# Optimization experiments

Measured on AMD Instinct MI355X. Metric: run time of the kernel, lower is better.

Reference implementation:

```python
import jax, jax.numpy as jnp
import numpy as np

D = 256      # d_model
NH = 8       # heads
NL = 3       # layers
DFF = 1024   # ffn hidden
WIN = 64     # attention window
EPS = 1e-5


def _sin_pos_embed(L, d):
    # Sinusoidal positional embedding, matches _create_pos_embedding.
    pos = jnp.arange(L, dtype=jnp.float32)[:, None]
    div = jnp.exp(jnp.arange(0, d, 2, dtype=jnp.float32) * (-np.log(10000.0) / d))
    pe = jnp.zeros((L, d), jnp.float32)
    pe = pe.at[:, 0::2].set(jnp.sin(pos * div))
    pe = pe.at[:, 1::2].set(jnp.cos(pos * div))
    return pe  # [L, D]


def _layer_norm(x, scale, bias):
    m = jnp.mean(x, axis=-1, keepdims=True)
    v = jnp.mean(jnp.square(x - m), axis=-1, keepdims=True)
    return (x - m) * jax.lax.rsqrt(v + EPS) * scale + bias


def _mha(x, Wi, bi, Wo, bo):
    # x: [N, S, D]; Wi: [3D, D]; Wo: [D, D]. torch nn.MultiheadAttention semantics (eval, no dropout).
    N, S, _ = x.shape
    dh = D // NH
    qkv = x @ Wi.T + bi                       # [N, S, 3D]
    q, k, v = jnp.split(qkv, 3, axis=-1)
    q = q.reshape(N, S, NH, dh).transpose(0, 2, 1, 3) * (dh ** -0.5)
    k = k.reshape(N, S, NH, dh).transpose(0, 2, 1, 3)
    v = v.reshape(N, S, NH, dh).transpose(0, 2, 1, 3)
    attn = jax.nn.softmax(jnp.einsum('nhqd,nhkd->nhqk', q, k), axis=-1)
    out = jnp.einsum('nhqk,nhkd->nhqd', attn, v)
    out = out.transpose(0, 2, 1, 3).reshape(N, S, D)
    return out @ Wo.T + bo


def setup_inputs() -> dict:
    key = jax.random.key(0)
    ks = jax.random.split(key, 16)
    s = 0.02
    return {
        'features': jax.random.normal(ks[0], (32, D, 32, 32), jnp.float32),
        'in_proj_w': jax.random.normal(ks[1], (NL, 3 * D, D), jnp.float32) * s,
        'in_proj_b': jnp.zeros((NL, 3 * D), jnp.float32),
        'out_proj_w': jax.random.normal(ks[2], (NL, D, D), jnp.float32) * s,
        'out_proj_b': jnp.zeros((NL, D), jnp.float32),
        'w1': jax.random.normal(ks[3], (NL, DFF, D), jnp.float32) * s,
        'b1': jnp.zeros((NL, DFF), jnp.float32),
        'w2': jax.random.normal(ks[4], (NL, D, DFF), jnp.float32) * s,
        'b2': jnp.zeros((NL, D), jnp.float32),
        'ln1_s': jnp.ones((NL, D), jnp.float32),
        'ln1_b': jnp.zeros((NL, D), jnp.float32),
        'ln2_s': jnp.ones((NL, D), jnp.float32),
        'ln2_b': jnp.zeros((NL, D), jnp.float32),
        'fnorm_s': jnp.ones((D,), jnp.float32),
        'fnorm_b': jnp.zeros((D,), jnp.float32),
    }


def reference(features, in_proj_w, in_proj_b, out_proj_w, out_proj_b,
              w1, b1, w2, b2, ln1_s, ln1_b, ln2_s, ln2_b, fnorm_s, fnorm_b):
    B, C, H, W = features.shape
    L = H * W
    x = features.reshape(B, C, L).transpose(0, 2, 1)   # [B, L, D]
    x = x + _sin_pos_embed(L, D)[None]                 # L == 1024 == max_len, no interp
    nw = L // WIN                                      # non-overlapping windows
    for i in range(NL):
        # windowed self-attention: all windows batched in one MHA call
        xw = x.reshape(B * nw, WIN, D)
        att = _mha(xw, in_proj_w[i], in_proj_b[i], out_proj_w[i], out_proj_b[i])
        att = att.reshape(B, L, D)
        x = _layer_norm(x + att, ln1_s[i], ln1_b[i])
        h = jax.nn.gelu(x @ w1[i].T + b1[i], approximate=False) @ w2[i].T + b2[i]
        x = _layer_norm(x + h, ln2_s[i], ln2_b[i])
    x = _layer_norm(x, fnorm_s, fnorm_b)
    return x.transpose(0, 2, 1).reshape(B, C, H, W)
```

## Files before the change

### kernel.cpp

```cpp
#include <hip/hip_runtime.h>
#include <hip/hip_bf16.h>

#define BSZ 32
#define DM 256
#define LSEQ 1024
#define MTOK (BSZ * LSEQ)
#define NHEAD 8
#define DHEAD 32
#define WIN 64
#define DFF 1024
#define M8 ((size_t)MTOK * 8)

typedef short bf16x8 __attribute__((ext_vector_type(8)));
typedef float f32x4 __attribute__((ext_vector_type(4)));
typedef unsigned short u16x8 __attribute__((ext_vector_type(8)));

union BF { __hip_bfloat16 h; unsigned short u; };
__device__ __forceinline__ unsigned short f2bf(float f) { BF b; b.h = __float2bfloat16(f); return b.u; }
__device__ __forceinline__ float bf2f(unsigned short u) { return __uint_as_float((unsigned)u << 16); }

#define GLD_LDS16(gp, lp) __builtin_amdgcn_global_load_lds( \
    (const __attribute__((address_space(1))) void*)(gp),    \
    (__attribute__((address_space(3))) void*)(lp), 16, 0, 0)

__device__ __forceinline__ float gelu_fast(float x) {
    float t = x * (0.7978845608f + 0.0356774081f * x * x);
    return x / (1.0f + __expf(-2.0f * t));
}

__global__ __launch_bounds__(256) void cvt_kernel(
    const float* __restrict__ s, unsigned short* __restrict__ d,
    int N, int K, int nl)
{
    int K8 = K >> 3;
    int per = N * K8;
    int c = blockIdx.x * 256 + threadIdx.x;
    if (c >= per * nl) return;
    int layer = c / per, rem = c - layer * per;
    int n = rem / K8, kc = rem - n * K8;
    const float* sp = s + (size_t)layer * N * K + (size_t)n * K + kc * 8;
    float4 v0 = *(const float4*)sp, v1 = *(const float4*)(sp + 4);
    uint4 o;
    o.x = f2bf(v0.x) | ((unsigned)f2bf(v0.y) << 16);
    o.y = f2bf(v0.z) | ((unsigned)f2bf(v0.w) << 16);
    o.z = f2bf(v1.x) | ((unsigned)f2bf(v1.y) << 16);
    o.w = f2bf(v1.z) | ((unsigned)f2bf(v1.w) << 16);
    *(uint4*)(d + (size_t)layer * N * K + (size_t)kc * N * 8 + (size_t)n * 8) = o;
}

__global__ __launch_bounds__(256) void pe_kernel(float* __restrict__ PE)
{
    int l = blockIdx.x, c = threadIdx.x;
    int i2 = c & ~1;
    float div = expf(-9.210340371976184f * (float)i2 / 256.0f);
    float ang = (float)l * div;
    PE[l * DM + c] = (c & 1) ? cosf(ang) : sinf(ang);
}

__global__ __launch_bounds__(256) void embed_kernel(
    const float* __restrict__ F, const float* __restrict__ PE,
    float* __restrict__ Xf, unsigned short* __restrict__ Xb)
{
    __shared__ float tile[64][65];
    int b = blockIdx.z, l0 = blockIdx.y * 64, c0 = blockIdx.x * 64;
    int tid = threadIdx.x;
    int li = tid & 63, c4 = tid >> 6;
    #pragma unroll
    for (int it = 0; it < 16; ++it) {
        int c = c4 + it * 4;
        tile[c][li] = F[((size_t)(b * DM + c0 + c)) * LSEQ + l0 + li];
    }
    __syncthreads();
    int ci = tid & 63, l4 = tid >> 6;
    #pragma unroll
    for (int it = 0; it < 16; ++it) {
        int l = l4 + it * 4;
        float x = tile[ci][l] + PE[(l0 + l) * DM + c0 + ci];
        Xf[((size_t)b * LSEQ + l0 + l) * DM + c0 + ci] = x;
    }
    int ch = tid >> 5;
    int lx = tid & 31;
    #pragma unroll
    for (int rd = 0; rd < 2; ++rd) {
        int l = lx + rd * 32;
        unsigned short vs[8];
        #pragma unroll
        for (int e = 0; e < 8; ++e) {
            int c = ch * 8 + e;
            vs[e] = f2bf(tile[c][l] + PE[(l0 + l) * DM + c0 + c]);
        }
        uint4 o;
        o.x = vs[0] | ((unsigned)vs[1] << 16);
        o.y = vs[2] | ((unsigned)vs[3] << 16);
        o.z = vs[4] | ((unsigned)vs[5] << 16);
        o.w = vs[6] | ((unsigned)vs[7] << 16);
        *(uint4*)(Xb + ((size_t)((c0 >> 3) + ch)) * M8 +
                  (size_t)(b * LSEQ + l0 + l) * 8) = o;
    }
}

__global__ __launch_bounds__(256) void gemm_mfma_kernel(
    const unsigned short* __restrict__ A, const unsigned short* __restrict__ Bw,
    const float* __restrict__ bias, unsigned short* __restrict__ Cb,
    int M, int N, int K, int gelu)
{
    const int tid = threadIdx.x;
    const int lane = tid & 63, wave = tid >> 6;
    const int l15 = lane & 15, quad = lane >> 4;
    const int wm = (wave & 1) * 64, wn = (wave >> 1) * 64;
    const int m0 = blockIdx.x * 128, n0 = blockIdx.y * 128;
    const size_t Ma8 = (size_t)M * 8, Nb8 = (size_t)N * 8;
    const size_t astep = 4 * Ma8, bstep = 4 * Nb8;

    const unsigned short* ap[4];
    const unsigned short* bp[4];
    #pragma unroll
    for (int i = 0; i < 4; ++i)
        ap[i] = A + quad * Ma8 + (size_t)(m0 + wm + i * 16 + l15) * 8;
    #pragma unroll
    for (int j = 0; j < 4; ++j)
        bp[j] = Bw + quad * Nb8 + (size_t)(n0 + wn + j * 16 + l15) * 8;

    f32x4 acc[4][4] = {};
    bf16x8 aA[4], bA[4], aB[4], bB[4];
    #pragma unroll
    for (int i = 0; i < 4; ++i) aA[i] = *(const bf16x8*)(ap[i]);
    #pragma unroll
    for (int j = 0; j < 4; ++j) bA[j] = *(const bf16x8*)(bp[j]);

    const int iters = K >> 5;
    for (int t = 0; t < iters; t += 2) {
        size_t o1 = (size_t)(t + 1);
        #pragma unroll
        for (int i = 0; i < 4; ++i) aB[i] = *(const bf16x8*)(ap[i] + o1 * astep);
        #pragma unroll
        for (int j = 0; j < 4; ++j) bB[j] = *(const bf16x8*)(bp[j] + o1 * bstep);
        #pragma unroll
        for (int i = 0; i < 4; ++i)
            #pragma unroll
            for (int j = 0; j < 4; ++j)
                acc[i][j] = __builtin_amdgcn_mfma_f32_16x16x32_bf16(
                    bA[j], aA[i], acc[i][j], 0, 0, 0);
        size_t o2 = (size_t)((t + 2 < iters) ? t + 2 : iters - 1);
        #pragma unroll
        for (int i = 0; i < 4; ++i) aA[i] = *(const bf16x8*)(ap[i] + o2 * astep);
        #pragma unroll
        for (int j = 0; j < 4; ++j) bA[j] = *(const bf16x8*)(bp[j] + o2 * bstep);
        #pragma unroll
        for (int i = 0; i < 4; ++i)
            #pragma unroll
            for (int j = 0; j < 4; ++j)
                acc[i][j] = __builtin_amdgcn_mfma_f32_16x16x32_bf16(
                    bB[j], aB[i], acc[i][j], 0, 0, 0);
    }

    float4 bb[4];
    #pragma unroll
    for (int j = 0; j < 4; ++j)
        bb[j] = *(const float4*)(bias + n0 + wn + j * 16 + quad * 4);

    #pragma unroll
    for (int i = 0; i < 4; ++i) {
        const size_t m8 = (size_t)(m0 + wm + i * 16 + l15) * 8;
        #pragma unroll
        for (int j = 0; j < 4; ++j) {
            int nb = n0 + wn + j * 16 + quad * 4;
            float v0 = acc[i][j][0] + bb[j].x;
            float v1 = acc[i][j][1] + bb[j].y;
            float v2 = acc[i][j][2] + bb[j].z;
            float v3 = acc[i][j][3] + bb[j].w;
            if (gelu) {
                v0 = gelu_fast(v0); v1 = gelu_fast(v1);
                v2 = gelu_fast(v2); v3 = gelu_fast(v3);
            }
            uint2 o;
            o.x = f2bf(v0) | ((unsigned)f2bf(v1) << 16);
            o.y = f2bf(v2) | ((unsigned)f2bf(v3) << 16);
            *(uint2*)(Cb + ((size_t)(nb >> 3)) * Ma8 + m8 + (nb & 7)) = o;
        }
    }
}

__global__ __launch_bounds__(256) void gemm_ln_kernel(
    const unsigned short* __restrict__ A, const unsigned short* __restrict__ Bw,
    const float* __restrict__ bias, const float* __restrict__ resid,
    const float* __restrict__ lns, const float* __restrict__ lnb,
    float* __restrict__ Xf, unsigned short* __restrict__ Xb, int K)
{
    __shared__ float Ss[256], Sq[256];
    const int tid = threadIdx.x;
    const int lane = tid & 63, wave = tid >> 6;
    const int l15 = lane & 15, quad = lane >> 4;
    const int wn = wave * 64;
    const int m0 = blockIdx.x * 64;
    const size_t Nb8 = (size_t)DM * 8;
    const size_t astep = 4 * M8, bstep = 4 * Nb8;

    const unsigned short* ap[4];
    const unsigned short* bp[4];
    #pragma unroll
    for (int i = 0; i < 4; ++i)
        ap[i] = A + quad * M8 + (size_t)(m0 + i * 16 + l15) * 8;
    #pragma unroll
    for (int j = 0; j < 4; ++j)
        bp[j] = Bw + quad * Nb8 + (size_t)(wn + j * 16 + l15) * 8;

    f32x4 acc[4][4] = {};
    bf16x8 aA[4], bA[4], aB[4], bB[4];
    #pragma unroll
    for (int i = 0; i < 4; ++i) aA[i] = *(const bf16x8*)(ap[i]);
    #pragma unroll
    for (int j = 0; j < 4; ++j) bA[j] = *(const bf16x8*)(bp[j]);

    const int iters = K >> 5;
    for (int t = 0; t < iters; t += 2) {
        size_t o1 = (size_t)(t + 1);
        #pragma unroll
        for (int i = 0; i < 4; ++i) aB[i] = *(const bf16x8*)(ap[i] + o1 * astep);
        #pragma unroll
        for (int j = 0; j < 4; ++j) bB[j] = *(const bf16x8*)(bp[j] + o1 * bstep);
        #pragma unroll
        for (int i = 0; i < 4; ++i)
            #pragma unroll
            for (int j = 0; j < 4; ++j)
                acc[i][j] = __builtin_amdgcn_mfma_f32_16x16x32_bf16(
                    bA[j], aA[i], acc[i][j], 0, 0, 0);
        size_t o2 = (size_t)((t + 2 < iters) ? t + 2 : iters - 1);
        #pragma unroll
        for (int i = 0; i < 4; ++i) aA[i] = *(const bf16x8*)(ap[i] + o2 * astep);
        #pragma unroll
        for (int j = 0; j < 4; ++j) bA[j] = *(const bf16x8*)(bp[j] + o2 * bstep);
        #pragma unroll
        for (int i = 0; i < 4; ++i)
            #pragma unroll
            for (int j = 0; j < 4; ++j)
                acc[i][j] = __builtin_amdgcn_mfma_f32_16x16x32_bf16(
                    bB[j], aB[i], acc[i][j], 0, 0, 0);
    }

    float4 bj[4];
    #pragma unroll
    for (int j = 0; j < 4; ++j)
        bj[j] = *(const float4*)(bias + wn + j * 16 + quad * 4);
    #pragma unroll
    for (int i = 0; i < 4; ++i) {
        const float* rp = resid + (size_t)(m0 + i * 16 + l15) * DM + wn + quad * 4;
        #pragma unroll
        for (int j = 0; j < 4; ++j) {
            float4 rr = *(const float4*)(rp + j * 16);
            acc[i][j][0] += bj[j].x + rr.x;
            acc[i][j][1] += bj[j].y + rr.y;
            acc[i][j][2] += bj[j].z + rr.z;
            acc[i][j][3] += bj[j].w + rr.w;
        }
    }

    #pragma unroll
    for (int i = 0; i < 4; ++i) {
        float s = 0.f, q = 0.f;
        #pragma unroll
        for (int j = 0; j < 4; ++j)
            #pragma unroll
            for (int r = 0; r < 4; ++r) {
                float x = acc[i][j][r];
                s += x; q = fmaf(x, x, q);
            }
        s += __shfl_xor(s, 16); q += __shfl_xor(q, 16);
        s += __shfl_xor(s, 32); q += __shfl_xor(q, 32);
        if (quad == 0) {
            Ss[wave * 64 + i * 16 + l15] = s;
            Sq[wave * 64 + i * 16 + l15] = q;
        }
    }
    __syncthreads();

    float4 scj[4], bbj[4];
    #pragma unroll
    for (int j = 0; j < 4; ++j) {
        scj[j] = *(const float4*)(lns + wn + j * 16 + quad * 4);
        bbj[j] = *(const float4*)(lnb + wn + j * 16 + quad * 4);
    }
    #pragma unroll
    for (int i = 0; i < 4; ++i) {
        int row = i * 16 + l15;
        float s = Ss[row] + Ss[64 + row] + Ss[128 + row] + Ss[192 + row];
        float q = Sq[row] + Sq[64 + row] + Sq[128 + row] + Sq[192 + row];
        float mean = s * (1.0f / 256.0f);
        float var  = q * (1.0f / 256.0f) - mean * mean;
        float rinv = rsqrtf(var + 1e-5f);
        #pragma unroll
        for (int j = 0; j < 4; ++j) {
            acc[i][j][0] = (acc[i][j][0] - mean) * rinv * scj[j].x + bbj[j].x;
            acc[i][j][1] = (acc[i][j][1] - mean) * rinv * scj[j].y + bbj[j].y;
            acc[i][j][2] = (acc[i][j][2] - mean) * rinv * scj[j].z + bbj[j].z;
            acc[i][j][3] = (acc[i][j][3] - mean) * rinv * scj[j].w + bbj[j].w;
        }
    }

    #pragma unroll
    for (int i = 0; i < 4; ++i) {
        int m = m0 + i * 16 + l15;
        size_t gf = (size_t)m * DM + wn + quad * 4;
        size_t m8 = (size_t)m * 8;
        #pragma unroll
        for (int j = 0; j < 4; ++j) {
            float4 o = { acc[i][j][0], acc[i][j][1], acc[i][j][2], acc[i][j][3] };
            *(float4*)(Xf + gf + j * 16) = o;
            int nb = wn + j * 16 + quad * 4;
            uint2 ob;
            ob.x = f2bf(o.x) | ((unsigned)f2bf(o.y) << 16);
            ob.y = f2bf(o.z) | ((unsigned)f2bf(o.w) << 16);
            *(uint2*)(Xb + ((size_t)(nb >> 3)) * M8 + m8 + (nb & 7)) = ob;
        }
    }
}

__global__ __launch_bounds__(256, 2) void ffn_fused_kernel(
    const unsigned short* __restrict__ A, const unsigned short* __restrict__ W1w,
    const float* __restrict__ b1, const unsigned short* __restrict__ W2w,
    const float* __restrict__ b2, const float* __restrict__ resid,
    const float* __restrict__ lns, const float* __restrict__ lnb,
    float* __restrict__ Xf, unsigned short* __restrict__ Xb)
{
    __shared__ unsigned short Hlds[16384];
    __shared__ float Ss[256], Sq[256];
    const int tid = threadIdx.x;
    const int lane = tid & 63, wave = tid >> 6;
    const int l15 = lane & 15, quad = lane >> 4;
    const int wn = wave * 64;
    const int m0 = blockIdx.x * 64;
    const size_t N1b8 = (size_t)DFF * 8;
    const size_t astep = 4 * M8, b1step = 4 * N1b8;

    const unsigned short* ap[4];
    #pragma unroll
    for (int i = 0; i < 4; ++i)
        ap[i] = A + quad * M8 + (size_t)(m0 + i * 16 + l15) * 8;

    f32x4 acc2[4][4] = {};

    for (int qq = 0; qq < 4; ++qq) {
        const unsigned short* bp[4];
        #pragma unroll
        for (int j = 0; j < 4; ++j)
            bp[j] = W1w + quad * N1b8 + (size_t)(qq * 256 + wn + j * 16 + l15) * 8;

        f32x4 acc1[4][4] = {};
        {
            bf16x8 aA[4], bA[4], aB[4], bB[4];
            #pragma unroll
            for (int i = 0; i < 4; ++i) aA[i] = *(const bf16x8*)(ap[i]);
            #pragma unroll
            for (int j = 0; j < 4; ++j) bA[j] = *(const bf16x8*)(bp[j]);
            for (int t = 0; t < 8; t += 2) {
                size_t o1 = (size_t)(t + 1);
                #pragma unroll
                for (int i = 0; i < 4; ++i) aB[i] = *(const bf16x8*)(ap[i] + o1 * astep);
                #pragma unroll
                for (int j = 0; j < 4; ++j) bB[j] = *(const bf16x8*)(bp[j] + o1 * b1step);
                #pragma unroll
                for (int i = 0; i < 4; ++i)
                    #pragma unroll
                    for (int j = 0; j < 4; ++j)
                        acc1[i][j] = __builtin_amdgcn_mfma_f32_16x16x32_bf16(
                            bA[j], aA[i], acc1[i][j], 0, 0, 0);
                size_t o2 = (size_t)((t + 2 < 8) ? t + 2 : 7);
                #pragma unroll
                for (int i = 0; i < 4; ++i) aA[i] = *(const bf16x8*)(ap[i] + o2 * astep);
                #pragma unroll
                for (int j = 0; j < 4; ++j) bA[j] = *(const bf16x8*)(bp[j] + o2 * b1step);
                #pragma unroll
                for (int i = 0; i < 4; ++i)
                    #pragma unroll
                    for (int j = 0; j < 4; ++j)
                        acc1[i][j] = __builtin_amdgcn_mfma_f32_16x16x32_bf16(
                            bB[j], aB[i], acc1[i][j], 0, 0, 0);
            }
        }
        {
            float4 bb[4];
            #pragma unroll
            for (int j = 0; j < 4; ++j)
                bb[j] = *(const float4*)(b1 + qq * 256 + wn + j * 16 + quad * 4);
            #pragma unroll
            for (int i = 0; i < 4; ++i) {
                int m = i * 16 + l15;
                #pragma unroll
                for (int j = 0; j < 4; ++j) {
                    float v0 = gelu_fast(acc1[i][j][0] + bb[j].x);
                    float v1 = gelu_fast(acc1[i][j][1] + bb[j].y);
                    float v2 = gelu_fast(acc1[i][j][2] + bb[j].z);
                    float v3 = gelu_fast(acc1[i][j][3] + bb[j].w);
                    int chunk = wave * 8 + j * 2 + (quad >> 1);
                    uint2 o;
                    o.x = f2bf(v0) | ((unsigned)f2bf(v1) << 16);
                    o.y = f2bf(v2) | ((unsigned)f2bf(v3) << 16);
                    *(uint2*)(Hlds + chunk * 512 + m * 8 + (quad & 1) * 4) = o;
                }
            }
        }
        __syncthreads();

        {
            const unsigned short* b2p[4];
            #pragma unroll
            for (int j = 0; j < 4; ++j)
                b2p[j] = W2w + ((size_t)(qq * 32 + quad)) * 2048 +
                         (size_t)(wn + j * 16 + l15) * 8;
            bf16x8 hA[4], w2A[4], w2B[4];
            #pragma unroll
            for (int j = 0; j < 4; ++j) w2A[j] = *(const bf16x8*)(b2p[j]);
            for (int t = 0; t < 8; t += 2) {
                size_t o1 = (size_t)(t + 1);
                #pragma unroll
                for (int j = 0; j < 4; ++j)
                    w2B[j] = *(const bf16x8*)(b2p[j] + o1 * 8192);
                #pragma unroll
                for (int i = 0; i < 4; ++i)
                    hA[i] = *(const bf16x8*)(Hlds + (t * 4 + quad) * 512 +
                                             (i * 16 + l15) * 8);
                #pragma unroll
                for (int i = 0; i < 4; ++i)
                    #pragma unroll
                    for (int j = 0; j < 4; ++j)
                        acc2[i][j] = __builtin_amdgcn_mfma_f32_16x16x32_bf16(
                            w2A[j], hA[i], acc2[i][j], 0, 0, 0);
                size_t o2 = (size_t)((t + 2 < 8) ? t + 2 : 7);
                #pragma unroll
                for (int j = 0; j < 4; ++j)
                    w2A[j] = *(const bf16x8*)(b2p[j] + o2 * 8192);
                #pragma unroll
                for (int i = 0; i < 4; ++i)
                    hA[i] = *(const bf16x8*)(Hlds + ((t + 1) * 4 + quad) * 512 +
                                             (i * 16 + l15) * 8);
                #pragma unroll
                for (int i = 0; i < 4; ++i)
                    #pragma unroll
                    for (int j = 0; j < 4; ++j)
                        acc2[i][j] = __builtin_amdgcn_mfma_f32_16x16x32_bf16(
                            w2B[j], hA[i], acc2[i][j], 0, 0, 0);
            }
        }
        __syncthreads();
    }

    float4 bj[4];
    #pragma unroll
    for (int j = 0; j < 4; ++j)
        bj[j] = *(const float4*)(b2 + wn + j * 16 + quad * 4);
    #pragma unroll
    for (int i = 0; i < 4; ++i) {
        const float* rp = resid + (size_t)(m0 + i * 16 + l15) * DM + wn + quad * 4;
        #pragma unroll
        for (int j = 0; j < 4; ++j) {
            float4 rr = *(const float4*)(rp + j * 16);
            acc2[i][j][0] += bj[j].x + rr.x;
            acc2[i][j][1] += bj[j].y + rr.y;
            acc2[i][j][2] += bj[j].z + rr.z;
            acc2[i][j][3] += bj[j].w + rr.w;
        }
    }

    #pragma unroll
    for (int i = 0; i < 4; ++i) {
        float s = 0.f, q = 0.f;
        #pragma unroll
        for (int j = 0; j < 4; ++j)
            #pragma unroll
            for (int r = 0; r < 4; ++r) {
                float x = acc2[i][j][r];
                s += x; q = fmaf(x, x, q);
            }
        s += __shfl_xor(s, 16); q += __shfl_xor(q, 16);
        s += __shfl_xor(s, 32); q += __shfl_xor(q, 32);
        if (quad == 0) {
            Ss[wave * 64 + i * 16 + l15] = s;
            Sq[wave * 64 + i * 16 + l15] = q;
        }
    }
    __syncthreads();

    float4 scj[4], bbj[4];
    #pragma unroll
    for (int j = 0; j < 4; ++j) {
        scj[j] = *(const float4*)(lns + wn + j * 16 + quad * 4);
        bbj[j] = *(const float4*)(lnb + wn + j * 16 + quad * 4);
    }
    #pragma unroll
    for (int i = 0; i < 4; ++i) {
        int row = i * 16 + l15;
        float s = Ss[row] + Ss[64 + row] + Ss[128 + row] + Ss[192 + row];
        float q = Sq[row] + Sq[64 + row] + Sq[128 + row] + Sq[192 + row];
        float mean = s * (1.0f / 256.0f);
        float var  = q * (1.0f / 256.0f) - mean * mean;
        float rinv = rsqrtf(var + 1e-5f);
        #pragma unroll
        for (int j = 0; j < 4; ++j) {
            acc2[i][j][0] = (acc2[i][j][0] - mean) * rinv * scj[j].x + bbj[j].x;
            acc2[i][j][1] = (acc2[i][j][1] - mean) * rinv * scj[j].y + bbj[j].y;
            acc2[i][j][2] = (acc2[i][j][2] - mean) * rinv * scj[j].z + bbj[j].z;
            acc2[i][j][3] = (acc2[i][j][3] - mean) * rinv * scj[j].w + bbj[j].w;
        }
    }

    #pragma unroll
    for (int i = 0; i < 4; ++i) {
        int m = m0 + i * 16 + l15;
        size_t gf = (size_t)m * DM + wn + quad * 4;
        size_t m8 = (size_t)m * 8;
        #pragma unroll
        for (int j = 0; j < 4; ++j) {
            float4 o = { acc2[i][j][0], acc2[i][j][1], acc2[i][j][2], acc2[i][j][3] };
            *(float4*)(Xf + gf + j * 16) = o;
            int nb = wn + j * 16 + quad * 4;
            uint2 ob;
            ob.x = f2bf(o.x) | ((unsigned)f2bf(o.y) << 16);
            ob.y = f2bf(o.z) | ((unsigned)f2bf(o.w) << 16);
            *(uint2*)(Xb + ((size_t)(nb >> 3)) * M8 + m8 + (nb & 7)) = ob;
        }
    }
}

__global__ __launch_bounds__(64) void attn_mfma_kernel(
    const unsigned short* __restrict__ QKV, unsigned short* __restrict__ ATT)
{
    __shared__ __align__(16) char smem[22016];
    unsigned short* Qs = (unsigned short*)smem;
    unsigned short* Ks = (unsigned short*)(smem + 4096);
    unsigned short* VT = (unsigned short*)(smem + 8192);
    unsigned short* Ps = (unsigned short*)(smem + 12800);
    float*          Po = (float*)(smem + 12800);

    const int wg = blockIdx.x, h = blockIdx.y;
    const int base = wg * WIN;
    const int lane = threadIdx.x;
    const int l15 = lane & 15, quad = lane >> 4;
    const float scale = 0.17677669529663687f;

    #pragma unroll
    for (int dc = 0; dc < 4; ++dc) {
        GLD_LDS16(QKV + ((size_t)(h * 4 + dc)) * M8 + (size_t)(base + lane) * 8,
                  Qs + dc * 512 + (size_t)lane * 8);
        GLD_LDS16(QKV + ((size_t)(32 + h * 4 + dc)) * M8 + (size_t)(base + lane) * 8,
                  Ks + dc * 512 + (size_t)lane * 8);
    }
    u16x8 vv[4];
    #pragma unroll
    for (int cc = 0; cc < 4; ++cc)
        vv[cc] = *(const u16x8*)(QKV + ((size_t)(64 + h * 4 + cc)) * M8 +
                                 (size_t)(base + lane) * 8);
    #pragma unroll
    for (int cc = 0; cc < 4; ++cc)
        #pragma unroll
        for (int e = 0; e < 8; ++e)
            VT[(cc * 8 + e) * 72 + lane] = vv[cc][e];
    __syncthreads();

    const f32x4 zero4 = {0.f, 0.f, 0.f, 0.f};
    bf16x8 aq[4], bk[4];
    #pragma unroll
    for (int i = 0; i < 4; ++i)
        aq[i] = *(const bf16x8*)(Qs + quad * 512 + (i * 16 + l15) * 8);
    #pragma unroll
    for (int j = 0; j < 4; ++j)
        bk[j] = *(const bf16x8*)(Ks + quad * 512 + (j * 16 + l15) * 8);
    f32x4 S[4][4];
    #pragma unroll
    for (int i = 0; i < 4; ++i)
        #pragma unroll
        for (int j = 0; j < 4; ++j)
            S[i][j] = __builtin_amdgcn_mfma_f32_16x16x32_bf16(aq[i], bk[j], zero4, 0, 0, 0);

    float mx[4][4], sum[4][4];
    #pragma unroll
    for (int i = 0; i < 4; ++i)
        #pragma unroll
        for (int r = 0; r < 4; ++r) {
            float m0 = -1e30f;
            #pragma unroll
            for (int j = 0; j < 4; ++j) {
                S[i][j][r] *= scale;
                m0 = fmaxf(m0, S[i][j][r]);
            }
            mx[i][r] = m0;
        }
    #pragma unroll
    for (int off = 1; off < 16; off <<= 1)
        #pragma unroll
        for (int i = 0; i < 4; ++i)
            #pragma unroll
            for (int r = 0; r < 4; ++r)
                mx[i][r] = fmaxf(mx[i][r], __shfl_xor(mx[i][r], off));
    #pragma unroll
    for (int i = 0; i < 4; ++i)
        #pragma unroll
        for (int r = 0; r < 4; ++r) {
            float s0 = 0.f;
            #pragma unroll
            for (int j = 0; j < 4; ++j) {
                float e = __expf(S[i][j][r] - mx[i][r]);
                S[i][j][r] = e;
                s0 += e;
            }
            sum[i][r] = s0;
        }
    #pragma unroll
    for (int off = 1; off < 16; off <<= 1)
        #pragma unroll
        for (int i = 0; i < 4; ++i)
            #pragma unroll
            for (int r = 0; r < 4; ++r)
                sum[i][r] += __shfl_xor(sum[i][r], off);

    #pragma unroll
    for (int i = 0; i < 4; ++i)
        #pragma unroll
        for (int r = 0; r < 4; ++r) {
            float inv = 1.0f / sum[i][r];
            #pragma unroll
            for (int j = 0; j < 4; ++j)
                Ps[(i * 16 + quad * 4 + r) * 72 + j * 16 + l15] =
                    f2bf(S[i][j][r] * inv);
        }
    asm volatile("s_waitcnt lgkmcnt(0)" ::: "memory");

    bf16x8 ap0[4], ap1[4], bv0[2], bv1[2];
    #pragma unroll
    for (int i = 0; i < 4; ++i) {
        ap0[i] = *(const bf16x8*)(Ps + (i * 16 + l15) * 72 + quad * 8);
        ap1[i] = *(const bf16x8*)(Ps + (i * 16 + l15) * 72 + 32 + quad * 8);
    }
    #pragma unroll
    for (int jd = 0; jd < 2; ++jd) {
        bv0[jd] = *(const bf16x8*)(VT + (jd * 16 + l15) * 72 + quad * 8);
        bv1[jd] = *(const bf16x8*)(VT + (jd * 16 + l15) * 72 + 32 + quad * 8);
    }
    f32x4 O[4][2];
    #pragma unroll
    for (int i = 0; i < 4; ++i)
        #pragma unroll
        for (int jd = 0; jd < 2; ++jd) {
            f32x4 t = __builtin_amdgcn_mfma_f32_16x16x32_bf16(ap0[i], bv0[jd], zero4, 0, 0, 0);
            O[i][jd] = __builtin_amdgcn_mfma_f32_16x16x32_bf16(ap1[i], bv1[jd], t, 0, 0, 0);
        }
    asm volatile("s_waitcnt lgkmcnt(0)" ::: "memory");

    #pragma unroll
    for (int i = 0; i < 4; ++i)
        #pragma unroll
        for (int jd = 0; jd < 2; ++jd)
            #pragma unroll
            for (int r = 0; r < 4; ++r)
                Po[(i * 16 + quad * 4 + r) * 36 + jd * 16 + l15] = O[i][jd][r];
    asm volatile("s_waitcnt lgkmcnt(0)" ::: "memory");

    #pragma unroll
    for (int g = 0; g < 4; ++g) {
        f32x4 t0 = *(const f32x4*)(Po + lane * 36 + g * 8);
        f32x4 t1 = *(const f32x4*)(Po + lane * 36 + g * 8 + 4);
        uint4 w;
        w.x = f2bf(t0[0]) | ((unsigned)f2bf(t0[1]) << 16);
        w.y = f2bf(t0[2]) | ((unsigned)f2bf(t0[3]) << 16);
        w.z = f2bf(t1[0]) | ((unsigned)f2bf(t1[1]) << 16);
        w.w = f2bf(t1[2]) | ((unsigned)f2bf(t1[3]) << 16);
        *(uint4*)(ATT + ((size_t)(h * 4 + g)) * M8 + (size_t)(base + lane) * 8) = w;
    }
}

__global__ __launch_bounds__(256) void out_ln_kernel(
    const float* __restrict__ Xf, const float* __restrict__ sc,
    const float* __restrict__ bi, float* __restrict__ out)
{
    __shared__ float tile[64][257];
    __shared__ float mean_s[64], rinv_s[64];
    int b = blockIdx.y, l0 = blockIdx.x * 64;
    int tid = threadIdx.x, wave = tid >> 6, lane = tid & 63;
    int c = lane * 4;
    #pragma unroll
    for (int it = 0; it < 16; ++it) {
        int tl = wave * 16 + it;
        float4 v = *(const float4*)(Xf + ((size_t)(b * LSEQ + l0 + tl)) * DM + c);
        *(float4*)&tile[tl][c] = v;
        float sm = v.x + v.y + v.z + v.w;
        float sq = v.x * v.x + v.y * v.y + v.z * v.z + v.w * v.w;
        #pragma unroll
        for (int off = 32; off > 0; off >>= 1) {
            sm += __shfl_down(sm, off);
            sq += __shfl_down(sq, off);
        }
        if (lane == 0) {
            float mean = sm * (1.0f / 256.0f);
            float var  = sq * (1.0f / 256.0f) - mean * mean;
            mean_s[tl] = mean;
            rinv_s[tl] = rsqrtf(var + 1e-5f);
        }
    }
    __syncthreads();
    int lout = tid & 63, crow = tid >> 6;
    #pragma unroll
    for (int ct = 0; ct < 4; ++ct) {
        int c0 = ct * 64;
        #pragma unroll
        for (int it = 0; it < 16; ++it) {
            int cc = c0 + crow + it * 4;
            float v = tile[lout][cc];
            out[((size_t)(b * DM + cc)) * LSEQ + l0 + lout] =
                (v - mean_s[lout]) * rinv_s[lout] * sc[cc] + bi[cc];
        }
    }
}

extern "C" void kernel_launch(void* const* d_in, const int* in_sizes, int n_in,
                              void* d_out, int out_size, void* d_ws, size_t ws_size,
                              hipStream_t stream)
{
    const float* F   = (const float*)d_in[0];
    const float* Wi  = (const float*)d_in[1];
    const float* Bi  = (const float*)d_in[2];
    const float* Wo  = (const float*)d_in[3];
    const float* Bo  = (const float*)d_in[4];
    const float* W1  = (const float*)d_in[5];
    const float* B1  = (const float*)d_in[6];
    const float* W2  = (const float*)d_in[7];
    const float* B2  = (const float*)d_in[8];
    const float* L1s = (const float*)d_in[9];
    const float* L1b = (const float*)d_in[10];
    const float* L2s = (const float*)d_in[11];
    const float* L2b = (const float*)d_in[12];
    const float* Fs  = (const float*)d_in[13];
    const float* Fb  = (const float*)d_in[14];

    char* w = (char*)d_ws;
    float*          Xf   = (float*)w;
    unsigned short* QKVb = (unsigned short*)(w + 33554432);
    unsigned short* Hb   = (unsigned short*)(w + 83886080);
    unsigned short* Xb   = (unsigned short*)(w + 150994944);
    unsigned short* ATTb = (unsigned short*)(w + 167772160);
    unsigned short* WB   = (unsigned short*)(w + 184549376);
    float*          PE   = (float*)(w + 189267968);
    unsigned short* Wib  = WB;
    unsigned short* Wob  = WB + 589824;
    unsigned short* W1b  = WB + 786432;
    unsigned short* W2b  = WB + 1572864;
    (void)Hb;

    cvt_kernel<<<(3 * 768 * 32 + 255) / 256, 256, 0, stream>>>(Wi, Wib, 768, 256, 3);
    cvt_kernel<<<(3 * 256 * 32 + 255) / 256, 256, 0, stream>>>(Wo, Wob, 256, 256, 3);
    cvt_kernel<<<(3 * 1024 * 32 + 255) / 256, 256, 0, stream>>>(W1, W1b, 1024, 256, 3);
    cvt_kernel<<<(3 * 256 * 128 + 255) / 256, 256, 0, stream>>>(W2, W2b, 256, 1024, 3);
    pe_kernel<<<LSEQ, 256, 0, stream>>>(PE);
    embed_kernel<<<dim3(DM / 64, LSEQ / 64, BSZ), 256, 0, stream>>>(F, PE, Xf, Xb);

    for (int i = 0; i < 3; ++i) {
        gemm_mfma_kernel<<<dim3(MTOK / 128, 768 / 128), 256, 0, stream>>>(
            Xb, Wib + (size_t)i * 196608, Bi + i * 768, QKVb, MTOK, 768, DM, 0);
        attn_mfma_kernel<<<dim3(BSZ * (LSEQ / WIN), NHEAD), 64, 0, stream>>>(QKVb, ATTb);
        gemm_ln_kernel<<<MTOK / 64, 256, 0, stream>>>(
            ATTb, Wob + (size_t)i * 65536, Bo + i * DM, Xf,
            L1s + i * DM, L1b + i * DM, Xf, Xb, DM);
        ffn_fused_kernel<<<MTOK / 64, 256, 0, stream>>>(
            Xb, W1b + (size_t)i * 262144, B1 + i * DFF,
            W2b + (size_t)i * 262144, B2 + i * DM, Xf,
            L2s + i * DM, L2b + i * DM, Xf, Xb);
    }

    out_ln_kernel<<<dim3(LSEQ / 64, BSZ), 256, 0, stream>>>(
        Xf, Fs, Fb, (float*)d_out);
}
```

Baseline: 646.3 us.

## Split fused FFN across 8 waves with double-buffered hidden LDS tile

The fused FFN kernel now launches 512 threads: the 64-row tile is split between two wave groups, so each wave holds half as many accumulators. This cuts register pressure and allows more waves per CU to hide global-load latency. The GELU hidden tile in LDS is double-buffered, which removes the second barrier per 256-column chunk. In exchange, the manual A/B register prefetch pipelining is dropped in favour of simple unrolled loops, each wave re-reads the same weight fragments for fewer rows, and LDS use grows.

```diff
diff --git a/kernel.cpp b/kernel.cpp
--- a/kernel.cpp
+++ b/kernel.cpp
@@ -315,87 +315,75 @@
     }
 }
 
-__global__ __launch_bounds__(256, 2) void ffn_fused_kernel(
+__global__ __launch_bounds__(512, 4) void ffn_fused_kernel(
     const unsigned short* __restrict__ A, const unsigned short* __restrict__ W1w,
     const float* __restrict__ b1, const unsigned short* __restrict__ W2w,
     const float* __restrict__ b2, const float* __restrict__ resid,
     const float* __restrict__ lns, const float* __restrict__ lnb,
     float* __restrict__ Xf, unsigned short* __restrict__ Xb)
 {
-    __shared__ unsigned short Hlds[16384];
+    __shared__ unsigned short Hlds[2][16384];
     __shared__ float Ss[256], Sq[256];
     const int tid = threadIdx.x;
     const int lane = tid & 63, wave = tid >> 6;
     const int l15 = lane & 15, quad = lane >> 4;
-    const int wn = wave * 64;
+    const int wh = wave >> 2;
+    const int wq = wave & 3;
+    const int wn = wq * 64;
     const int m0 = blockIdx.x * 64;
     const size_t N1b8 = (size_t)DFF * 8;
     const size_t astep = 4 * M8, b1step = 4 * N1b8;
 
-    const unsigned short* ap[4];
-    #pragma unroll
-    for (int i = 0; i < 4; ++i)
-        ap[i] = A + quad * M8 + (size_t)(m0 + i * 16 + l15) * 8;
-
-    f32x4 acc2[4][4] = {};
+    const unsigned short* ap0 = A + quad * M8 + (size_t)(m0 + wh * 32 + l15) * 8;
+    const unsigned short* ap1 = ap0 + 16 * 8;
+
+    f32x4 acc2[2][4] = {};
 
     for (int qq = 0; qq < 4; ++qq) {
+        unsigned short* Hbuf = Hlds[qq & 1];
         const unsigned short* bp[4];
         #pragma unroll
         for (int j = 0; j < 4; ++j)
             bp[j] = W1w + quad * N1b8 + (size_t)(qq * 256 + wn + j * 16 + l15) * 8;
 
-        f32x4 acc1[4][4] = {};
-        {
-            bf16x8 aA[4], bA[4], aB[4], bB[4];
-            #pragma unroll
-            for (int i = 0; i < 4; ++i) aA[i] = *(const bf16x8*)(ap[i]);
-            #pragma unroll
-            for (int j = 0; j < 4; ++j) bA[j] = *(const bf16x8*)(bp[j]);
-            for (int t = 0; t < 8; t += 2) {
-                size_t o1 = (size_t)(t + 1);
-                #pragma unroll
-                for (int i = 0; i < 4; ++i) aB[i] = *(const bf16x8*)(ap[i] + o1 * astep);
-                #pragma unroll
-                for (int j = 0; j < 4; ++j) bB[j] = *(const bf16x8*)(bp[j] + o1 * b1step);
-                #pragma unroll
-                for (int i = 0; i < 4; ++i)
-                    #pragma unroll
-                    for (int j = 0; j < 4; ++j)
-                        acc1[i][j] = __builtin_amdgcn_mfma_f32_16x16x32_bf16(
-                            bA[j], aA[i], acc1[i][j], 0, 0, 0);
-                size_t o2 = (size_t)((t + 2 < 8) ? t + 2 : 7);
-                #pragma unroll
-                for (int i = 0; i < 4; ++i) aA[i] = *(const bf16x8*)(ap[i] + o2 * astep);
-                #pragma unroll
-                for (int j = 0; j < 4; ++j) bA[j] = *(const bf16x8*)(bp[j] + o2 * b1step);
-                #pragma unroll
-                for (int i = 0; i < 4; ++i)
-                    #pragma unroll
-                    for (int j = 0; j < 4; ++j)
-                        acc1[i][j] = __builtin_amdgcn_mfma_f32_16x16x32_bf16(
-                            bB[j], aB[i], acc1[i][j], 0, 0, 0);
-            }
-        }
+        f32x4 acc1[2][4] = {};
+        #pragma unroll
+        for (int t = 0; t < 8; ++t) {
+            bf16x8 a0 = *(const bf16x8*)(ap0 + (size_t)t * astep);
+            bf16x8 a1 = *(const bf16x8*)(ap1 + (size_t)t * astep);
+            bf16x8 w0 = *(const bf16x8*)(bp[0] + (size_t)t * b1step);
+            bf16x8 w1 = *(const bf16x8*)(bp[1] + (size_t)t * b1step);
+            bf16x8 w2 = *(const bf16x8*)(bp[2] + (size_t)t * b1step);
+            bf16x8 w3 = *(const bf16x8*)(bp[3] + (size_t)t * b1step);
+            acc1[0][0] = __builtin_amdgcn_mfma_f32_16x16x32_bf16(w0, a0, acc1[0][0], 0, 0, 0);
+            acc1[0][1] = __builtin_amdgcn_mfma_f32_16x16x32_bf16(w1, a0, acc1[0][1], 0, 0, 0);
+            acc1[0][2] = __builtin_amdgcn_mfma_f32_16x16x32_bf16(w2, a0, acc1[0][2], 0, 0, 0);
+            acc1[0][3] = __builtin_amdgcn_mfma_f32_16x16x32_bf16(w3, a0, acc1[0][3], 0, 0, 0);
+            acc1[1][0] = __builtin_amdgcn_mfma_f32_16x16x32_bf16(w0, a1, acc1[1][0], 0, 0, 0);
+            acc1[1][1] = __builtin_amdgcn_mfma_f32_16x16x32_bf16(w1, a1, acc1[1][1], 0, 0, 0);
+            acc1[1][2] = __builtin_amdgcn_mfma_f32_16x16x32_bf16(w2, a1, acc1[1][2], 0, 0, 0);
+            acc1[1][3] = __builtin_amdgcn_mfma_f32_16x16x32_bf16(w3, a1, acc1[1][3], 0, 0, 0);
+        }
+
         {
             float4 bb[4];
             #pragma unroll
             for (int j = 0; j < 4; ++j)
                 bb[j] = *(const float4*)(b1 + qq * 256 + wn + j * 16 + quad * 4);
             #pragma unroll
-            for (int i = 0; i < 4; ++i) {
-                int m = i * 16 + l15;
+            for (int i = 0; i < 2; ++i) {
+                int m = wh * 32 + i * 16 + l15;
                 #pragma unroll
                 for (int j = 0; j < 4; ++j) {
                     float v0 = gelu_fast(acc1[i][j][0] + bb[j].x);
                     float v1 = gelu_fast(acc1[i][j][1] + bb[j].y);
                     float v2 = gelu_fast(acc1[i][j][2] + bb[j].z);
                     float v3 = gelu_fast(acc1[i][j][3] + bb[j].w);
-                    int chunk = wave * 8 + j * 2 + (quad >> 1);
+                    int chunk = wq * 8 + j * 2 + (quad >> 1);
                     uint2 o;
                     o.x = f2bf(v0) | ((unsigned)f2bf(v1) << 16);
                     o.y = f2bf(v2) | ((unsigned)f2bf(v3) << 16);
-                    *(uint2*)(Hlds + chunk * 512 + m * 8 + (quad & 1) * 4) = o;
+                    *(uint2*)(Hbuf + chunk * 512 + m * 8 + (quad & 1) * 4) = o;
                 }
             }
         }
@@ -407,41 +395,26 @@
             for (int j = 0; j < 4; ++j)
                 b2p[j] = W2w + ((size_t)(qq * 32 + quad)) * 2048 +
                          (size_t)(wn + j * 16 + l15) * 8;
-            bf16x8 hA[4], w2A[4], w2B[4];
-            #pragma unroll
-            for (int j = 0; j < 4; ++j) w2A[j] = *(const bf16x8*)(b2p[j]);
-            for (int t = 0; t < 8; t += 2) {
-                size_t o1 = (size_t)(t + 1);
-                #pragma unroll
-                for (int j = 0; j < 4; ++j)
-                    w2B[j] = *(const bf16x8*)(b2p[j] + o1 * 8192);
-                #pragma unroll
-                for (int i = 0; i < 4; ++i)
-                    hA[i] = *(const bf16x8*)(Hlds + (t * 4 + quad) * 512 +
-                                             (i * 16 + l15) * 8);
-                #pragma unroll
-                for (int i = 0; i < 4; ++i)
-                    #pragma unroll
-                    for (int j = 0; j < 4; ++j)
-                        acc2[i][j] = __builtin_amdgcn_mfma_f32_16x16x32_bf16(
-                            w2A[j], hA[i], acc2[i][j], 0, 0, 0);
-                size_t o2 = (size_t)((t + 2 < 8) ? t + 2 : 7);
-                #pragma unroll
-                for (int j = 0; j < 4; ++j)
-                    w2A[j] = *(const bf16x8*)(b2p[j] + o2 * 8192);
-                #pragma unroll
-                for (int i = 0; i < 4; ++i)
-                    hA[i] = *(const bf16x8*)(Hlds + ((t + 1) * 4 + quad) * 512 +
-                                             (i * 16 + l15) * 8);
-                #pragma unroll
-                for (int i = 0; i < 4; ++i)
-                    #pragma unroll
-                    for (int j = 0; j < 4; ++j)
-                        acc2[i][j] = __builtin_amdgcn_mfma_f32_16x16x32_bf16(
-                            w2B[j], hA[i], acc2[i][j], 0, 0, 0);
+            #pragma unroll
+            for (int t = 0; t < 8; ++t) {
+                bf16x8 h0 = *(const bf16x8*)(Hbuf + (t * 4 + quad) * 512 +
+                                             (wh * 32 + l15) * 8);
+                bf16x8 h1 = *(const bf16x8*)(Hbuf + (t * 4 + quad) * 512 +
+                                             (wh * 32 + 16 + l15) * 8);
+                bf16x8 w0 = *(const bf16x8*)(b2p[0] + (size_t)t * 8192);
+                bf16x8 w1 = *(const bf16x8*)(b2p[1] + (size_t)t * 8192);
+                bf16x8 w2 = *(const bf16x8*)(b2p[2] + (size_t)t * 8192);
+                bf16x8 w3 = *(const bf16x8*)(b2p[3] + (size_t)t * 8192);
+                acc2[0][0] = __builtin_amdgcn_mfma_f32_16x16x32_bf16(w0, h0, acc2[0][0], 0, 0, 0);
+                acc2[0][1] = __builtin_amdgcn_mfma_f32_16x16x32_bf16(w1, h0, acc2[0][1], 0, 0, 0);
+                acc2[0][2] = __builtin_amdgcn_mfma_f32_16x16x32_bf16(w2, h0, acc2[0][2], 0, 0, 0);
+                acc2[0][3] = __builtin_amdgcn_mfma_f32_16x16x32_bf16(w3, h0, acc2[0][3], 0, 0, 0);
+                acc2[1][0] = __builtin_amdgcn_mfma_f32_16x16x32_bf16(w0, h1, acc2[1][0], 0, 0, 0);
+                acc2[1][1] = __builtin_amdgcn_mfma_f32_16x16x32_bf16(w1, h1, acc2[1][1], 0, 0, 0);
+                acc2[1][2] = __builtin_amdgcn_mfma_f32_16x16x32_bf16(w2, h1, acc2[1][2], 0, 0, 0);
+                acc2[1][3] = __builtin_amdgcn_mfma_f32_16x16x32_bf16(w3, h1, acc2[1][3], 0, 0, 0);
             }
         }
-        __syncthreads();
     }
 
     float4 bj[4];
@@ -449,8 +422,8 @@
     for (int j = 0; j < 4; ++j)
         bj[j] = *(const float4*)(b2 + wn + j * 16 + quad * 4);
     #pragma unroll
-    for (int i = 0; i < 4; ++i) {
-        const float* rp = resid + (size_t)(m0 + i * 16 + l15) * DM + wn + quad * 4;
+    for (int i = 0; i < 2; ++i) {
+        const float* rp = resid + (size_t)(m0 + wh * 32 + i * 16 + l15) * DM + wn + quad * 4;
         #pragma unroll
         for (int j = 0; j < 4; ++j) {
             float4 rr = *(const float4*)(rp + j * 16);
@@ -462,7 +435,7 @@
     }
 
     #pragma unroll
-    for (int i = 0; i < 4; ++i) {
+    for (int i = 0; i < 2; ++i) {
         float s = 0.f, q = 0.f;
         #pragma unroll
         for (int j = 0; j < 4; ++j)
@@ -474,8 +447,8 @@
         s += __shfl_xor(s, 16); q += __shfl_xor(q, 16);
         s += __shfl_xor(s, 32); q += __shfl_xor(q, 32);
         if (quad == 0) {
-            Ss[wave * 64 + i * 16 + l15] = s;
-            Sq[wave * 64 + i * 16 + l15] = q;
+            Ss[wq * 64 + wh * 32 + i * 16 + l15] = s;
+            Sq[wq * 64 + wh * 32 + i * 16 + l15] = q;
         }
     }
     __syncthreads();
@@ -487,8 +460,8 @@
         bbj[j] = *(const float4*)(lnb + wn + j * 16 + quad * 4);
     }
     #pragma unroll
-    for (int i = 0; i < 4; ++i) {
-        int row = i * 16 + l15;
+    for (int i = 0; i < 2; ++i) {
+        int row = wh * 32 + i * 16 + l15;
         float s = Ss[row] + Ss[64 + row] + Ss[128 + row] + Ss[192 + row];
         float q = Sq[row] + Sq[64 + row] + Sq[128 + row] + Sq[192 + row];
         float mean = s * (1.0f / 256.0f);
@@ -504,8 +477,8 @@
     }
 
     #pragma unroll
-    for (int i = 0; i < 4; ++i) {
-        int m = m0 + i * 16 + l15;
+    for (int i = 0; i < 2; ++i) {
+        int m = m0 + wh * 32 + i * 16 + l15;
         size_t gf = (size_t)m * DM + wn + quad * 4;
         size_t m8 = (size_t)m * 8;
         #pragma unroll
@@ -733,7 +706,6 @@
     char* w = (char*)d_ws;
     float*          Xf   = (float*)w;
     unsigned short* QKVb = (unsigned short*)(w + 33554432);
-    unsigned short* Hb   = (unsigned short*)(w + 83886080);
     unsigned short* Xb   = (unsigned short*)(w + 150994944);
     unsigned short* ATTb = (unsigned short*)(w + 167772160);
     unsigned short* WB   = (unsigned short*)(w + 184549376);
@@ -742,7 +714,6 @@
     unsigned short* Wob  = WB + 589824;
     unsigned short* W1b  = WB + 786432;
     unsigned short* W2b  = WB + 1572864;
-    (void)Hb;
 
     cvt_kernel<<<(3 * 768 * 32 + 255) / 256, 256, 0, stream>>>(Wi, Wib, 768, 256, 3);
     cvt_kernel<<<(3 * 256 * 32 + 255) / 256, 256, 0, stream>>>(Wo, Wob, 256, 256, 3);
@@ -758,7 +729,7 @@
         gemm_ln_kernel<<<MTOK / 64, 256, 0, stream>>>(
             ATTb, Wob + (size_t)i * 65536, Bo + i * DM, Xf,
             L1s + i * DM, L1b + i * DM, Xf, Xb, DM);
-        ffn_fused_kernel<<<MTOK / 64, 256, 0, stream>>>(
+        ffn_fused_kernel<<<MTOK / 64, 512, 0, stream>>>(
             Xb, W1b + (size_t)i * 262144, B1 + i * DFF,
             W2b + (size_t)i * 262144, B2 + i * DM, Xf,
             L2s + i * DM, L2b + i * DM, Xf, Xb);
```

After: 619.9 us. 1.04x faster.
